# Kernel optimization log

Hardware: AMD Instinct MI355X
Metric: run time of the kernel (lower is better)

Reference implementation:

```python
import jax, jax.numpy as jnp
import numpy as np

N, S, F, E, H, O, L, FE = 8, 1024, 64, 512, 8, 64, 6, 4
HD = E // H
FF = FE * E


def setup_inputs() -> dict:
    key = jax.random.key(0)
    ks = iter(jax.random.split(key, 40))
    def rn(shape, s=0.02):
        return jax.random.normal(next(ks), shape, jnp.float32) * s
    return {
        'x': jax.random.normal(next(ks), (N, F, S), jnp.float32),
        'W_first': rn((F, E)), 'b_first': jnp.zeros((E,), jnp.float32),
        'pos_emb': rn((S, E)),
        'Wq': rn((L, HD, HD)), 'bq': jnp.zeros((L, HD), jnp.float32),
        'Wk': rn((L, HD, HD)), 'bk': jnp.zeros((L, HD), jnp.float32),
        'Wv': rn((L, HD, HD)), 'bv': jnp.zeros((L, HD), jnp.float32),
        'Wo': rn((L, E, E)), 'bo': jnp.zeros((L, E), jnp.float32),
        'g1': jnp.ones((L, E), jnp.float32), 'be1': jnp.zeros((L, E), jnp.float32),
        'Wf1': rn((L, E, FF)), 'bf1': jnp.zeros((L, FF), jnp.float32),
        'Wf2': rn((L, FF, E)), 'bf2': jnp.zeros((L, E), jnp.float32),
        'g2': jnp.ones((L, E), jnp.float32), 'be2': jnp.zeros((L, E), jnp.float32),
        'Wfin': rn((E, O)), 'bfin': jnp.zeros((O,), jnp.float32),
    }


def layernorm(x, g, b, eps=1e-5):
    m = jnp.mean(x, axis=-1, keepdims=True)
    v = jnp.mean(jnp.square(x - m), axis=-1, keepdims=True)
    return (x - m) * jax.lax.rsqrt(v + eps) * g + b


def reference(x, W_first, b_first, pos_emb, Wq, bq, Wk, bk, Wv, bv, Wo, bo,
              g1, be1, Wf1, bf1, Wf2, bf2, g2, be2, Wfin, bfin):
    # x: (N, F, S) -> (N, S, F)
    h = jax.nn.relu(jnp.einsum('nfs,fe->nse', x, W_first) + b_first) + pos_emb[None]
    scale = E ** 0.5  # note: module scales by sqrt(embed_size), not sqrt(head_dim)
    for i in range(L):
        t = h.reshape(N, S, H, HD)
        q = jnp.einsum('nshd,de->nshe', t, Wq[i]) + bq[i]
        k = jnp.einsum('nshd,de->nshe', t, Wk[i]) + bk[i]
        v = jnp.einsum('nshd,de->nshe', t, Wv[i]) + bv[i]
        energy = jnp.einsum('nqhd,nkhd->nhqk', q, k)  # (N,H,S,S)
        att = jax.nn.softmax(energy / scale, axis=-1)
        o = jnp.einsum('nhqk,nkhd->nqhd', att, v).reshape(N, S, E)
        o = jnp.einsum('nse,ef->nsf', o, Wo[i]) + bo[i]
        hx = layernorm(o + h, g1[i], be1[i])
        ff = jax.nn.relu(jnp.einsum('nse,ef->nsf', hx, Wf1[i]) + bf1[i])
        ff = jnp.einsum('nsf,fe->nse', ff, Wf2[i]) + bf2[i]
        h = layernorm(ff + hx, g2[i], be2[i])
    # Conv1d kernel_size=1 == pointwise linear over channels; output (N, O, S)
    return jnp.einsum('nse,eo->nos', h, Wfin) + bfin[None, :, None]
```

## Files before the change

kernel.cpp:

```cpp
#include <hip/hip_runtime.h>
#include <hip/hip_bf16.h>
#include <math.h>

#define N_ 8
#define S_ 1024
#define F_ 64
#define E_ 512
#define H_ 8
#define O_ 64
#define L_ 6
#define HD_ 64
#define FF_ 2048
#define SCALE_ 0.044194173824159216f
#define LOG2E_ 1.4426950408889634f
#define QSCALE_ (SCALE_ * LOG2E_)

typedef unsigned short u16;
typedef __attribute__((ext_vector_type(8))) unsigned short u16x8;
typedef __attribute__((ext_vector_type(8))) short short8;
typedef __attribute__((ext_vector_type(4))) float floatx4;

__device__ __forceinline__ u16 f2b(float f) {
    union { float f; unsigned u; } v; v.f = f;
    unsigned u = v.u;
    unsigned r = (u + 0x7FFFu + ((u >> 16) & 1u)) >> 16;
    return (u16)r;
}
__device__ __forceinline__ u16 f2b_fast(float f) {
    union { float f; unsigned u; } v; v.f = f;
    return (u16)((v.u + 0x8000u) >> 16);
}
__device__ __forceinline__ float b2f(u16 h) {
    union { unsigned u; float f; } v; v.u = ((unsigned)h) << 16;
    return v.f;
}
__device__ __forceinline__ int pperm(int row) {
    return ((2 * (row >> 2) + 5 * (row & 3)) & 7) | ((row & 2) << 2);
}

__global__ __launch_bounds__(256) void first_mfma(
    const float* __restrict__ x, const u16* __restrict__ wt,
    const float* __restrict__ bf, const float* __restrict__ pe,
    u16* __restrict__ resb)
{
    __shared__ u16 a_s[128][72];
    int t = threadIdx.x;
    int w = t >> 6, lane = t & 63, quad = lane >> 4, c16 = lane & 15;
    int rowhalf = w >> 1, colhalf = w & 1;
    int col0 = blockIdx.x * 128;
    int row0 = blockIdx.y * 128;
    int n = row0 >> 10, s0 = row0 & 1023;

    const float* xb = x + (size_t)n * F_ * S_ + s0;
    #pragma unroll
    for (int i = 0; i < 8; i++) {
        int pos = (t + i * 256) * 4;
        int f = pos >> 7, sl = pos & 127;
        float4 v = *(const float4*)&xb[(size_t)f * S_ + sl];
        a_s[sl + 0][f] = f2b_fast(v.x);
        a_s[sl + 1][f] = f2b_fast(v.y);
        a_s[sl + 2][f] = f2b_fast(v.z);
        a_s[sl + 3][f] = f2b_fast(v.w);
    }
    __syncthreads();

    floatx4 acc[4][4];
    #pragma unroll
    for (int mt = 0; mt < 4; mt++)
        #pragma unroll
        for (int nt = 0; nt < 4; nt++) acc[mt][nt] = (floatx4){0.f, 0.f, 0.f, 0.f};

    #pragma unroll
    for (int ks = 0; ks < 2; ks++) {
        short8 af[4], bfr[4];
        #pragma unroll
        for (int mt = 0; mt < 4; mt++)
            af[mt] = *(const short8*)&a_s[rowhalf * 64 + mt * 16 + c16][ks * 32 + quad * 8];
        #pragma unroll
        for (int nt = 0; nt < 4; nt++)
            bfr[nt] = *(const short8*)&wt[(size_t)(col0 + colhalf * 64 + nt * 16 + c16) * F_
                                          + ks * 32 + quad * 8];
        #pragma unroll
        for (int mt = 0; mt < 4; mt++)
            #pragma unroll
            for (int nt = 0; nt < 4; nt++)
                acc[mt][nt] = __builtin_amdgcn_mfma_f32_16x16x32_bf16(
                    af[mt], bfr[nt], acc[mt][nt], 0, 0, 0);
    }

    #pragma unroll
    for (int nt = 0; nt < 4; nt++) {
        int col = col0 + colhalf * 64 + nt * 16 + c16;
        float bv = bf[col];
        #pragma unroll
        for (int mt = 0; mt < 4; mt++) {
            #pragma unroll
            for (int r = 0; r < 4; r++) {
                size_t row = (size_t)row0 + rowhalf * 64 + mt * 16 + quad * 4 + r;
                int s = (int)(row & 1023);
                float v = fmaxf(acc[mt][nt][r] + bv, 0.f) + pe[(size_t)s * E_ + col];
                resb[row * E_ + col] = f2b_fast(v);
            }
        }
    }
}

__global__ __launch_bounds__(256) void wcast_t(
    const float* __restrict__ W0, u16* __restrict__ Wt0, int K, int Nc)
{
    __shared__ float tile[32][33];
    int t = threadIdx.x;
    int bx = blockIdx.x, by = blockIdx.y;
    const float* W = W0 + (size_t)blockIdx.z * K * Nc;
    u16* Wt = Wt0 + (size_t)blockIdx.z * K * Nc;
    #pragma unroll
    for (int i = 0; i < 4; i++) {
        int q = t + i * 256; int r = q >> 5, c = q & 31;
        tile[r][c] = W[(size_t)(by * 32 + r) * Nc + bx * 32 + c];
    }
    __syncthreads();
    #pragma unroll
    for (int i = 0; i < 4; i++) {
        int q = t + i * 256; int r = q >> 5, c = q & 31;
        Wt[(size_t)(bx * 32 + r) * K + by * 32 + c] = f2b(tile[c][r]);
    }
}

__global__ __launch_bounds__(256) void qkvw_cast(
    const float* __restrict__ Wq, const float* __restrict__ Wk,
    const float* __restrict__ Wv,
    u16* __restrict__ wqt, u16* __restrict__ wkt, u16* __restrict__ wvt)
{
    int l = blockIdx.x;
    int t = threadIdx.x;
    size_t off = (size_t)l * HD_ * HD_;
    #pragma unroll
    for (int i = 0; i < 16; i++) {
        int idx = t + i * 256;
        int e = idx >> 6, d = idx & 63;
        wqt[off + idx] = f2b(Wq[off + d * HD_ + e]);
        wkt[off + idx] = f2b(Wk[off + d * HD_ + e]);
        wvt[off + idx] = f2b(Wv[off + d * HD_ + e]);
    }
}

__global__ __launch_bounds__(256) void qkv_mfma(
    const u16* __restrict__ hb,
    const u16* __restrict__ wqt, const u16* __restrict__ wkt,
    const u16* __restrict__ wvt,
    const float* __restrict__ bq, const float* __restrict__ bk,
    const float* __restrict__ bv,
    u16* __restrict__ qo, u16* __restrict__ ko, u16* __restrict__ vo)
{
    __shared__ u16 a_s[256][72];
    int t = threadIdx.x;
    int w = t >> 6, lane = t & 63, quad = lane >> 4, c16 = lane & 15;
    size_t row0 = (size_t)blockIdx.x * 256;

    #pragma unroll
    for (int i = 0; i < 8; i++) {
        int q = t + i * 256; int r = q >> 3, c = q & 7;
        *(u16x8*)&a_s[r][c * 8] = *(const u16x8*)&hb[(row0 + r) * HD_ + c * 8];
    }
    __syncthreads();

    short8 af[4][2];
    #pragma unroll
    for (int mt = 0; mt < 4; mt++)
        #pragma unroll
        for (int ks = 0; ks < 2; ks++)
            af[mt][ks] = *(const short8*)&a_s[w * 64 + mt * 16 + c16][ks * 32 + quad * 8];

    const u16* wts[3] = {wqt, wkt, wvt};
    const float* bs[3] = {bq, bk, bv};
    u16* outs[3] = {qo, ko, vo};

    #pragma unroll
    for (int m = 0; m < 3; m++) {
        short8 bfr[4][2];
        #pragma unroll
        for (int nt = 0; nt < 4; nt++)
            #pragma unroll
            for (int ks = 0; ks < 2; ks++)
                bfr[nt][ks] = *(const short8*)&wts[m][(nt * 16 + c16) * HD_ + ks * 32 + quad * 8];
        floatx4 acc[4][4];
        #pragma unroll
        for (int mt = 0; mt < 4; mt++)
            #pragma unroll
            for (int nt = 0; nt < 4; nt++) acc[mt][nt] = (floatx4){0.f, 0.f, 0.f, 0.f};
        #pragma unroll
        for (int ks = 0; ks < 2; ks++)
            #pragma unroll
            for (int mt = 0; mt < 4; mt++)
                #pragma unroll
                for (int nt = 0; nt < 4; nt++)
                    acc[mt][nt] = __builtin_amdgcn_mfma_f32_16x16x32_bf16(
                        af[mt][ks], bfr[nt][ks], acc[mt][nt], 0, 0, 0);
        float osc = (m == 0) ? QSCALE_ : 1.0f;
        #pragma unroll
        for (int nt = 0; nt < 4; nt++) {
            float bv_ = bs[m][nt * 16 + c16];
            #pragma unroll
            for (int mt = 0; mt < 4; mt++)
                #pragma unroll
                for (int r = 0; r < 4; r++)
                    outs[m][(row0 + w * 64 + mt * 16 + quad * 4 + r) * HD_ + nt * 16 + c16] =
                        f2b_fast((acc[mt][nt][r] + bv_) * osc);
        }
    }
}

__global__ __launch_bounds__(256) void vtrans(
    const u16* __restrict__ vb, u16* __restrict__ vt)
{
    int bid = blockIdx.x;
    int st = bid & 15, hh = (bid >> 4) & 7, n = bid >> 7;
    __shared__ u16 tile[64][72];
    int t = threadIdx.x;
    #pragma unroll
    for (int i = 0; i < 2; i++) {
        int q = t + i * 256; int sl = q >> 3, c = q & 7;
        *(u16x8*)&tile[sl][c * 8] =
            *(const u16x8*)&vb[(((size_t)(n * S_ + st * 64 + sl)) * H_ + hh) * 64 + c * 8];
    }
    __syncthreads();
    #pragma unroll
    for (int i = 0; i < 2; i++) {
        int q = t + i * 256; int d = q >> 3, sc = q & 7;
        u16x8 v;
        #pragma unroll
        for (int j = 0; j < 8; j++) v[j] = tile[sc * 8 + j][d];
        *(u16x8*)&vt[((size_t)(n * H_ + hh) * 64 + d) * (size_t)S_ + st * 64 + sc * 8] = v;
    }
}

__global__ __launch_bounds__(256, 2) void attn_mfma(
    const u16* __restrict__ Q, const u16* __restrict__ K,
    const u16* __restrict__ Vt, u16* __restrict__ O)
{
    int bid = blockIdx.x;
    int qt = bid & 15, hh = (bid >> 4) & 7, n = bid >> 7;
    int t = threadIdx.x;
    int w = t >> 6, lane = t & 63, quad = lane >> 4, c16 = lane & 15;

    __shared__ u16 qp_s[64][72];
    __shared__ u16 k_s[64][72];
    __shared__ u16 vt_s[64][72];
    u16 (*p_s)[72] = &qp_s[w * 16];

    const size_t qkbase = (size_t)n * S_ * E_ + hh * 64;
    const size_t vtbase = ((size_t)(n * H_ + hh) * 64) * (size_t)S_;

    #pragma unroll
    for (int i = 0; i < 2; i++) {
        int q = t + i * 256; int r = q >> 3, c = q & 7;
        *(u16x8*)&qp_s[r][c * 8] =
            *(const u16x8*)&Q[qkbase + (size_t)(qt * 64 + r) * E_ + c * 8];
    }
    __syncthreads();

    short8 af[2];
    #pragma unroll
    for (int ks = 0; ks < 2; ks++)
        af[ks] = *(const short8*)&qp_s[w * 16 + c16][ks * 32 + quad * 8];

    const short8 ones = {(short)0x3F80, (short)0x3F80, (short)0x3F80, (short)0x3F80,
                         (short)0x3F80, (short)0x3F80, (short)0x3F80, (short)0x3F80};
    const int pr = pperm(c16);
    int pw[4];
    #pragma unroll
    for (int r = 0; r < 4; r++) pw[r] = pperm(quad * 4 + r);

    floatx4 oacc[4], lacc;
    lacc = (floatx4){0.f, 0.f, 0.f, 0.f};
    #pragma unroll
    for (int nt = 0; nt < 4; nt++) oacc[nt] = (floatx4){0.f, 0.f, 0.f, 0.f};

    int ar = t >> 3, acq = (t & 7) * 8;
    u16x8 pk[2], pv[2];
    #pragma unroll
    for (int i = 0; i < 2; i++) {
        pk[i] = *(const u16x8*)&K[qkbase + (size_t)(ar + i * 32) * E_ + acq];
        pv[i] = *(const u16x8*)&Vt[vtbase + (size_t)(ar + i * 32) * S_ + acq];
    }

    for (int k0 = 0; k0 < S_; k0 += 64) {
        #pragma unroll
        for (int i = 0; i < 2; i++) {
            *(u16x8*)&k_s[ar + i * 32][acq] = pk[i];
            *(u16x8*)&vt_s[ar + i * 32][acq] = pv[i];
        }
        __syncthreads();
        if (k0 + 64 < S_) {
            #pragma unroll
            for (int i = 0; i < 2; i++) {
                pk[i] = *(const u16x8*)&K[qkbase + (size_t)(k0 + 64 + ar + i * 32) * E_ + acq];
                pv[i] = *(const u16x8*)&Vt[vtbase + (size_t)(ar + i * 32) * S_ + k0 + 64 + acq];
            }
        }

        floatx4 sc[4];
        #pragma unroll
        for (int nt = 0; nt < 4; nt++) sc[nt] = (floatx4){0.f, 0.f, 0.f, 0.f};
        #pragma unroll
        for (int ks = 0; ks < 2; ks++) {
            short8 bfr[4];
            #pragma unroll
            for (int nt = 0; nt < 4; nt++)
                bfr[nt] = *(const short8*)&k_s[nt * 16 + c16][ks * 32 + quad * 8];
            #pragma unroll
            for (int nt = 0; nt < 4; nt++)
                sc[nt] = __builtin_amdgcn_mfma_f32_16x16x32_bf16(af[ks], bfr[nt], sc[nt], 0, 0, 0);
        }

        #pragma unroll
        for (int nt = 0; nt < 4; nt++)
            #pragma unroll
            for (int r = 0; r < 4; r++)
                p_s[pw[r]][nt * 16 + c16] = f2b_fast(exp2f(sc[nt][r]));

        #pragma unroll
        for (int ks = 0; ks < 2; ks++) {
            short8 vf[4];
            #pragma unroll
            for (int nt = 0; nt < 4; nt++)
                vf[nt] = *(const short8*)&vt_s[nt * 16 + c16][ks * 32 + quad * 8];
            short8 pf = *(const short8*)&p_s[pr][ks * 32 + quad * 8];
            lacc = __builtin_amdgcn_mfma_f32_16x16x32_bf16(pf, ones, lacc, 0, 0, 0);
            #pragma unroll
            for (int nt = 0; nt < 4; nt++)
                oacc[nt] = __builtin_amdgcn_mfma_f32_16x16x32_bf16(pf, vf[nt], oacc[nt], 0, 0, 0);
        }
        __syncthreads();
    }

    #pragma unroll
    for (int r = 0; r < 4; r++) {
        float rl = 1.f / lacc[r];
        int s = qt * 64 + w * 16 + quad * 4 + r;
        size_t base = (size_t)(n * S_ + s) * E_ + hh * 64;
        #pragma unroll
        for (int nt = 0; nt < 4; nt++)
            O[base + nt * 16 + c16] = f2b_fast(oacc[nt][r] * rl);
    }
}

template <int MT, bool RELU, bool HASRES, bool OUTF32, bool OUTBF16>
__global__ __launch_bounds__(256, 2) void gemm_mfma(
    const u16* __restrict__ A, const u16* __restrict__ Bt,
    const float* __restrict__ bias, const u16* __restrict__ resid,
    float* __restrict__ outf, u16* __restrict__ outb, int M, int Nc, int K)
{
    constexpr int MTILES = MT / 32;
    __shared__ u16 a_s[MT][72];
    __shared__ u16 b_s[128][72];
    int t = threadIdx.x;
    int w = t >> 6, lane = t & 63, quad = lane >> 4, c16 = lane & 15;
    int rowhalf = w >> 1, colhalf = w & 1;
    size_t row0 = (size_t)blockIdx.y * MT;
    size_t col0 = (size_t)blockIdx.x * 128;

    floatx4 acc[MTILES][4];
    #pragma unroll
    for (int mt = 0; mt < MTILES; mt++)
        #pragma unroll
        for (int nt = 0; nt < 4; nt++) acc[mt][nt] = (floatx4){0.f, 0.f, 0.f, 0.f};

    int ar = t >> 3, acq = (t & 7) * 8;
    u16x8 pa[MTILES], pb[4];
    #pragma unroll
    for (int i = 0; i < MTILES; i++)
        pa[i] = *(const u16x8*)&A[(row0 + ar + i * 32) * K + acq];
    #pragma unroll
    for (int i = 0; i < 4; i++)
        pb[i] = *(const u16x8*)&Bt[(col0 + ar + i * 32) * K + acq];

    for (int k0 = 0; k0 < K; k0 += 64) {
        #pragma unroll
        for (int i = 0; i < MTILES; i++)
            *(u16x8*)&a_s[ar + i * 32][acq] = pa[i];
        #pragma unroll
        for (int i = 0; i < 4; i++)
            *(u16x8*)&b_s[ar + i * 32][acq] = pb[i];
        __syncthreads();
        if (k0 + 64 < K) {
            #pragma unroll
            for (int i = 0; i < MTILES; i++)
                pa[i] = *(const u16x8*)&A[(row0 + ar + i * 32) * K + k0 + 64 + acq];
            #pragma unroll
            for (int i = 0; i < 4; i++)
                pb[i] = *(const u16x8*)&Bt[(col0 + ar + i * 32) * K + k0 + 64 + acq];
        }
        #pragma unroll
        for (int ks = 0; ks < 2; ks++) {
            short8 af[MTILES], bf[4];
            #pragma unroll
            for (int mt = 0; mt < MTILES; mt++)
                af[mt] = *(const short8*)&a_s[rowhalf * (MT / 2) + mt * 16 + c16][ks * 32 + quad * 8];
            #pragma unroll
            for (int nt = 0; nt < 4; nt++)
                bf[nt] = *(const short8*)&b_s[colhalf * 64 + nt * 16 + c16][ks * 32 + quad * 8];
            #pragma unroll
            for (int mt = 0; mt < MTILES; mt++)
                #pragma unroll
                for (int nt = 0; nt < 4; nt++)
                    acc[mt][nt] = __builtin_amdgcn_mfma_f32_16x16x32_bf16(
                        af[mt], bf[nt], acc[mt][nt], 0, 0, 0);
        }
        __syncthreads();
    }

    #pragma unroll
    for (int nt = 0; nt < 4; nt++) {
        int col = (int)col0 + colhalf * 64 + nt * 16 + c16;
        float bv = bias[col];
        #pragma unroll
        for (int mt = 0; mt < MTILES; mt++) {
            size_t rowb = row0 + rowhalf * (MT / 2) + mt * 16 + quad * 4;
            #pragma unroll
            for (int r = 0; r < 4; r++) {
                size_t row = rowb + r;
                float v = acc[mt][nt][r] + bv;
                if constexpr (HASRES) v += b2f(resid[row * Nc + col]);
                if constexpr (RELU) v = fmaxf(v, 0.f);
                if constexpr (OUTF32) outf[row * Nc + col] = v;
                if constexpr (OUTBF16) outb[row * Nc + col] = f2b_fast(v);
            }
        }
    }
}

__global__ __launch_bounds__(256) void layernorm_k(
    const float* __restrict__ in, const float* __restrict__ g,
    const float* __restrict__ bb, u16* __restrict__ outb)
{
    int row = blockIdx.x;
    int t = threadIdx.x;
    const float* x = in + (size_t)row * E_;
    float x0 = x[t], x1 = x[t + 256];
    float s = x0 + x1;
    #pragma unroll
    for (int off = 32; off; off >>= 1) s += __shfl_down(s, off, 64);
    __shared__ float red[4];
    int wid = t >> 6, lane = t & 63;
    if (lane == 0) red[wid] = s;
    __syncthreads();
    float m = (red[0] + red[1] + red[2] + red[3]) * (1.f / E_);
    float d0 = x0 - m, d1 = x1 - m;
    float sq = d0 * d0 + d1 * d1;
    #pragma unroll
    for (int off = 32; off; off >>= 1) sq += __shfl_down(sq, off, 64);
    __syncthreads();
    if (lane == 0) red[wid] = sq;
    __syncthreads();
    float var = (red[0] + red[1] + red[2] + red[3]) * (1.f / E_);
    float rstd = rsqrtf(var + 1e-5f);
    outb[(size_t)row * E_ + t] = f2b_fast(d0 * rstd * g[t] + bb[t]);
    outb[(size_t)row * E_ + t + 256] = f2b_fast(d1 * rstd * g[t + 256] + bb[t + 256]);
}

__global__ __launch_bounds__(256) void final_mfma(
    const u16* __restrict__ hb, const u16* __restrict__ wft,
    const float* __restrict__ bfin, float* __restrict__ outp)
{
    __shared__ u16 a_s[64][72];
    int t = threadIdx.x;
    int w = t >> 6, lane = t & 63, quad = lane >> 4, c16 = lane & 15;
    size_t row0 = (size_t)blockIdx.x * 64;

    floatx4 acc[4];
    #pragma unroll
    for (int nt = 0; nt < 4; nt++) acc[nt] = (floatx4){0.f, 0.f, 0.f, 0.f};

    int ar = t >> 3, acq = (t & 7) * 8;
    u16x8 pa[2];
    #pragma unroll
    for (int i = 0; i < 2; i++)
        pa[i] = *(const u16x8*)&hb[(row0 + ar + i * 32) * E_ + acq];

    for (int k0 = 0; k0 < E_; k0 += 64) {
        #pragma unroll
        for (int i = 0; i < 2; i++)
            *(u16x8*)&a_s[ar + i * 32][acq] = pa[i];
        __syncthreads();
        if (k0 + 64 < E_) {
            #pragma unroll
            for (int i = 0; i < 2; i++)
                pa[i] = *(const u16x8*)&hb[(row0 + ar + i * 32) * E_ + k0 + 64 + acq];
        }
        #pragma unroll
        for (int ks = 0; ks < 2; ks++) {
            short8 af = *(const short8*)&a_s[w * 16 + c16][ks * 32 + quad * 8];
            #pragma unroll
            for (int nt = 0; nt < 4; nt++) {
                short8 bf = *(const short8*)&wft[(nt * 16 + c16) * E_ + k0 + ks * 32 + quad * 8];
                acc[nt] = __builtin_amdgcn_mfma_f32_16x16x32_bf16(af, bf, acc[nt], 0, 0, 0);
            }
        }
        __syncthreads();
    }

    #pragma unroll
    for (int nt = 0; nt < 4; nt++) {
        int o = nt * 16 + c16;
        float bv = bfin[o];
        #pragma unroll
        for (int r = 0; r < 4; r++) {
            size_t row = row0 + w * 16 + quad * 4 + r;
            int n = (int)(row >> 10), s = (int)(row & 1023);
            outp[((size_t)(n * O_ + o)) * S_ + s] = acc[nt][r] + bv;
        }
    }
}

extern "C" void kernel_launch(void* const* d_in, const int* in_sizes, int n_in,
                              void* d_out, int out_size, void* d_ws, size_t ws_size,
                              hipStream_t stream)
{
    const float* x       = (const float*)d_in[0];
    const float* W_first = (const float*)d_in[1];
    const float* b_first = (const float*)d_in[2];
    const float* pos_emb = (const float*)d_in[3];
    const float* Wq      = (const float*)d_in[4];
    const float* bq      = (const float*)d_in[5];
    const float* Wk      = (const float*)d_in[6];
    const float* bk      = (const float*)d_in[7];
    const float* Wv      = (const float*)d_in[8];
    const float* bv      = (const float*)d_in[9];
    const float* Wo      = (const float*)d_in[10];
    const float* bo      = (const float*)d_in[11];
    const float* g1      = (const float*)d_in[12];
    const float* be1     = (const float*)d_in[13];
    const float* Wf1     = (const float*)d_in[14];
    const float* bf1     = (const float*)d_in[15];
    const float* Wf2     = (const float*)d_in[16];
    const float* bf2     = (const float*)d_in[17];
    const float* g2      = (const float*)d_in[18];
    const float* be2     = (const float*)d_in[19];
    const float* Wfin    = (const float*)d_in[20];
    const float* bfin    = (const float*)d_in[21];
    float* out = (float*)d_out;

    const size_t M4 = (size_t)N_ * S_ * E_;
    float* t1   = (float*)d_ws;
    u16*   resb = (u16*)(t1 + M4);
    u16*   qb   = resb + M4;
    u16*   kb   = qb + M4;
    u16*   vb   = kb + M4;
    u16*   vt   = vb + M4;
    u16*   ob   = vt + M4;
    u16*   ffb  = qb;
    u16*   wot  = ob + M4;
    u16*   wf1t = wot + (size_t)L_ * E_ * E_;
    u16*   wf2t = wf1t + (size_t)L_ * E_ * FF_;
    u16*   wqt  = wf2t + (size_t)L_ * FF_ * E_;
    u16*   wkt  = wqt + (size_t)L_ * HD_ * HD_;
    u16*   wvt  = wkt + (size_t)L_ * HD_ * HD_;
    u16*   wft  = wvt + (size_t)L_ * HD_ * HD_;
    u16*   w1t  = wft + (size_t)O_ * E_;

    const int rows = N_ * S_;

    qkvw_cast<<<L_, 256, 0, stream>>>(Wq, Wk, Wv, wqt, wkt, wvt);
    wcast_t<<<dim3(E_ / 32, F_ / 32, 1), 256, 0, stream>>>(W_first, w1t, F_, E_);
    wcast_t<<<dim3(E_ / 32, E_ / 32, L_), 256, 0, stream>>>(Wo, wot, E_, E_);
    wcast_t<<<dim3(FF_ / 32, E_ / 32, L_), 256, 0, stream>>>(Wf1, wf1t, E_, FF_);
    wcast_t<<<dim3(E_ / 32, FF_ / 32, L_), 256, 0, stream>>>(Wf2, wf2t, FF_, E_);
    wcast_t<<<dim3(O_ / 32, E_ / 32, 1), 256, 0, stream>>>(Wfin, wft, E_, O_);

    first_mfma<<<dim3(E_ / 128, rows / 128), 256, 0, stream>>>(
        x, w1t, b_first, pos_emb, resb);

    for (int i = 0; i < L_; i++) {
        qkv_mfma<<<256, 256, 0, stream>>>(
            resb, wqt + (size_t)i * HD_ * HD_, wkt + (size_t)i * HD_ * HD_,
            wvt + (size_t)i * HD_ * HD_, bq + i * HD_, bk + i * HD_, bv + i * HD_,
            qb, kb, vb);
        vtrans<<<1024, 256, 0, stream>>>(vb, vt);
        attn_mfma<<<1024, 256, 0, stream>>>(qb, kb, vt, ob);
        gemm_mfma<64, false, true, true, false><<<dim3(E_ / 128, rows / 64), 256, 0, stream>>>(
            ob, wot + (size_t)i * E_ * E_, bo + i * E_, resb, t1, nullptr, rows, E_, E_);
        layernorm_k<<<rows, 256, 0, stream>>>(t1, g1 + i * E_, be1 + i * E_, resb);
        gemm_mfma<128, true, false, false, true><<<dim3(FF_ / 128, rows / 128), 256, 0, stream>>>(
            resb, wf1t + (size_t)i * E_ * FF_, bf1 + i * FF_, nullptr, nullptr, ffb,
            rows, FF_, E_);
        gemm_mfma<64, false, true, true, false><<<dim3(E_ / 128, rows / 64), 256, 0, stream>>>(
            ffb, wf2t + (size_t)i * FF_ * E_, bf2 + i * E_, resb, t1, nullptr,
            rows, E_, FF_);
        layernorm_k<<<rows, 256, 0, stream>>>(t1, g2 + i * E_, be2 + i * E_, resb);
    }

    final_mfma<<<rows / 64, 256, 0, stream>>>(resb, wft, bfin, out);
}
```

Before: 1.044 ms.

## Double attention query tile per block and compute transposed scores to drop P permutation

The attention kernel now handles 128 queries per block (32 per wave) instead of 64, so each K/V tile staged in shared memory is reused across twice as many queries and the grid halves to 512 blocks. Scores are computed transposed (K as the A operand, Q as B), so each lane holds four consecutive keys for one query and can write P with vectorized 4-wide stores. This removes the pperm row permutation and makes the output stores vectorized. It adds register pressure from doubled accumulators and lowers block count, which may reduce occupancy and load balance.

```diff
diff --git a/kernel.cpp b/kernel.cpp
--- a/kernel.cpp
+++ b/kernel.cpp
@@ -16,6 +16,7 @@
 #define QSCALE_ (SCALE_ * LOG2E_)
 
 typedef unsigned short u16;
+typedef __attribute__((ext_vector_type(4))) unsigned short u16x4;
 typedef __attribute__((ext_vector_type(8))) unsigned short u16x8;
 typedef __attribute__((ext_vector_type(8))) short short8;
 typedef __attribute__((ext_vector_type(4))) float floatx4;
@@ -33,9 +34,6 @@
 __device__ __forceinline__ float b2f(u16 h) {
     union { unsigned u; float f; } v; v.u = ((unsigned)h) << 16;
     return v.f;
-}
-__device__ __forceinline__ int pperm(int row) {
-    return ((2 * (row >> 2) + 5 * (row & 3)) & 7) | ((row & 2) << 2);
 }
 
 __global__ __launch_bounds__(256) void first_mfma(
@@ -239,42 +237,44 @@
     const u16* __restrict__ Vt, u16* __restrict__ O)
 {
     int bid = blockIdx.x;
-    int qt = bid & 15, hh = (bid >> 4) & 7, n = bid >> 7;
+    int qt = bid & 7, hh = (bid >> 3) & 7, n = bid >> 6;
     int t = threadIdx.x;
     int w = t >> 6, lane = t & 63, quad = lane >> 4, c16 = lane & 15;
 
-    __shared__ u16 qp_s[64][72];
+    __shared__ u16 qp_s[128][72];
     __shared__ u16 k_s[64][72];
     __shared__ u16 vt_s[64][72];
-    u16 (*p_s)[72] = &qp_s[w * 16];
+    u16 (*p_s)[72] = &qp_s[w * 32];
 
     const size_t qkbase = (size_t)n * S_ * E_ + hh * 64;
     const size_t vtbase = ((size_t)(n * H_ + hh) * 64) * (size_t)S_;
 
     #pragma unroll
-    for (int i = 0; i < 2; i++) {
+    for (int i = 0; i < 4; i++) {
         int q = t + i * 256; int r = q >> 3, c = q & 7;
         *(u16x8*)&qp_s[r][c * 8] =
-            *(const u16x8*)&Q[qkbase + (size_t)(qt * 64 + r) * E_ + c * 8];
-    }
-    __syncthreads();
-
-    short8 af[2];
-    #pragma unroll
-    for (int ks = 0; ks < 2; ks++)
-        af[ks] = *(const short8*)&qp_s[w * 16 + c16][ks * 32 + quad * 8];
+            *(const u16x8*)&Q[qkbase + (size_t)(qt * 128 + r) * E_ + c * 8];
+    }
+    __syncthreads();
+
+    short8 qf[2][2];
+    #pragma unroll
+    for (int nq = 0; nq < 2; nq++)
+        #pragma unroll
+        for (int ks = 0; ks < 2; ks++)
+            qf[nq][ks] = *(const short8*)&qp_s[w * 32 + nq * 16 + c16][ks * 32 + quad * 8];
 
     const short8 ones = {(short)0x3F80, (short)0x3F80, (short)0x3F80, (short)0x3F80,
                          (short)0x3F80, (short)0x3F80, (short)0x3F80, (short)0x3F80};
-    const int pr = pperm(c16);
-    int pw[4];
-    #pragma unroll
-    for (int r = 0; r < 4; r++) pw[r] = pperm(quad * 4 + r);
-
-    floatx4 oacc[4], lacc;
-    lacc = (floatx4){0.f, 0.f, 0.f, 0.f};
-    #pragma unroll
-    for (int nt = 0; nt < 4; nt++) oacc[nt] = (floatx4){0.f, 0.f, 0.f, 0.f};
+
+    floatx4 oaccT[4][2];
+    floatx4 lacc[2];
+    #pragma unroll
+    for (int nq = 0; nq < 2; nq++) {
+        lacc[nq] = (floatx4){0.f, 0.f, 0.f, 0.f};
+        #pragma unroll
+        for (int mt = 0; mt < 4; mt++) oaccT[mt][nq] = (floatx4){0.f, 0.f, 0.f, 0.f};
+    }
 
     int ar = t >> 3, acq = (t & 7) * 8;
     u16x8 pk[2], pv[2];
@@ -299,49 +299,69 @@
             }
         }
 
-        floatx4 sc[4];
-        #pragma unroll
-        for (int nt = 0; nt < 4; nt++) sc[nt] = (floatx4){0.f, 0.f, 0.f, 0.f};
+        floatx4 st[4][2];
+        #pragma unroll
+        for (int mt = 0; mt < 4; mt++)
+            #pragma unroll
+            for (int nq = 0; nq < 2; nq++) st[mt][nq] = (floatx4){0.f, 0.f, 0.f, 0.f};
         #pragma unroll
         for (int ks = 0; ks < 2; ks++) {
-            short8 bfr[4];
-            #pragma unroll
-            for (int nt = 0; nt < 4; nt++)
-                bfr[nt] = *(const short8*)&k_s[nt * 16 + c16][ks * 32 + quad * 8];
-            #pragma unroll
-            for (int nt = 0; nt < 4; nt++)
-                sc[nt] = __builtin_amdgcn_mfma_f32_16x16x32_bf16(af[ks], bfr[nt], sc[nt], 0, 0, 0);
-        }
-
-        #pragma unroll
-        for (int nt = 0; nt < 4; nt++)
-            #pragma unroll
-            for (int r = 0; r < 4; r++)
-                p_s[pw[r]][nt * 16 + c16] = f2b_fast(exp2f(sc[nt][r]));
+            short8 kf[4];
+            #pragma unroll
+            for (int mt = 0; mt < 4; mt++)
+                kf[mt] = *(const short8*)&k_s[mt * 16 + c16][ks * 32 + quad * 8];
+            #pragma unroll
+            for (int mt = 0; mt < 4; mt++)
+                #pragma unroll
+                for (int nq = 0; nq < 2; nq++)
+                    st[mt][nq] = __builtin_amdgcn_mfma_f32_16x16x32_bf16(
+                        kf[mt], qf[nq][ks], st[mt][nq], 0, 0, 0);
+        }
+
+        #pragma unroll
+        for (int nq = 0; nq < 2; nq++)
+            #pragma unroll
+            for (int mt = 0; mt < 4; mt++) {
+                u16x4 h;
+                #pragma unroll
+                for (int r = 0; r < 4; r++) h[r] = f2b_fast(exp2f(st[mt][nq][r]));
+                *(u16x4*)&p_s[nq * 16 + c16][mt * 16 + quad * 4] = h;
+            }
 
         #pragma unroll
         for (int ks = 0; ks < 2; ks++) {
+            short8 pf[2];
+            #pragma unroll
+            for (int nq = 0; nq < 2; nq++)
+                pf[nq] = *(const short8*)&p_s[nq * 16 + c16][ks * 32 + quad * 8];
             short8 vf[4];
             #pragma unroll
-            for (int nt = 0; nt < 4; nt++)
-                vf[nt] = *(const short8*)&vt_s[nt * 16 + c16][ks * 32 + quad * 8];
-            short8 pf = *(const short8*)&p_s[pr][ks * 32 + quad * 8];
-            lacc = __builtin_amdgcn_mfma_f32_16x16x32_bf16(pf, ones, lacc, 0, 0, 0);
-            #pragma unroll
-            for (int nt = 0; nt < 4; nt++)
-                oacc[nt] = __builtin_amdgcn_mfma_f32_16x16x32_bf16(pf, vf[nt], oacc[nt], 0, 0, 0);
+            for (int mt = 0; mt < 4; mt++)
+                vf[mt] = *(const short8*)&vt_s[mt * 16 + c16][ks * 32 + quad * 8];
+            #pragma unroll
+            for (int nq = 0; nq < 2; nq++) {
+                lacc[nq] = __builtin_amdgcn_mfma_f32_16x16x32_bf16(ones, pf[nq], lacc[nq], 0, 0, 0);
+                #pragma unroll
+                for (int mt = 0; mt < 4; mt++)
+                    oaccT[mt][nq] = __builtin_amdgcn_mfma_f32_16x16x32_bf16(
+                        vf[mt], pf[nq], oaccT[mt][nq], 0, 0, 0);
+            }
         }
         __syncthreads();
     }
 
     #pragma unroll
-    for (int r = 0; r < 4; r++) {
-        float rl = 1.f / lacc[r];
-        int s = qt * 64 + w * 16 + quad * 4 + r;
+    for (int nq = 0; nq < 2; nq++) {
+        float rl = 1.f / lacc[nq][0];
+        int s = qt * 128 + w * 32 + nq * 16 + c16;
         size_t base = (size_t)(n * S_ + s) * E_ + hh * 64;
         #pragma unroll
-        for (int nt = 0; nt < 4; nt++)
-            O[base + nt * 16 + c16] = f2b_fast(oacc[nt][r] * rl);
+        for (int mt = 0; mt < 4; mt++) {
+            u16x4 h;
+            #pragma unroll
+            for (int r = 0; r < 4; r++) h[r] = f2b_fast(oaccT[mt][nq][r] * rl);
+            *(u16x4*)&O[base + mt * 16 + quad * 4] = h;
+        }
     }
 }
 
@@ -577,7 +597,7 @@
             wvt + (size_t)i * HD_ * HD_, bq + i * HD_, bk + i * HD_, bv + i * HD_,
             qb, kb, vb);
         vtrans<<<1024, 256, 0, stream>>>(vb, vt);
-        attn_mfma<<<1024, 256, 0, stream>>>(qb, kb, vt, ob);
+        attn_mfma<<<512, 256, 0, stream>>>(qb, kb, vt, ob);
         gemm_mfma<64, false, true, true, false><<<dim3(E_ / 128, rows / 64), 256, 0, stream>>>(
             ob, wot + (size_t)i * E_ * E_, bo + i * E_, resb, t1, nullptr, rows, E_, E_);
         layernorm_k<<<rows, 256, 0, stream>>>(t1, g1 + i * E_, be1 + i * E_, resb);
```

New measurement: 1.020 ms. -2.3%, faster.
